# Kernel tuning notes

Measured on AMD Instinct MI355X. Metric: run time of the kernel, lower is better.

Reference implementation:

```python
import jax, jax.numpy as jnp
import numpy as np

N_NODES = 100000
N_EDGES = 1600000
NUM_FEATURES = 128
HIDDEN = 64
NUM_CLASSES = 2


def _gcn_norm(edge_index, num_nodes):
    # PyG gcn_norm: add self-loops, symmetric degree normalization.
    loop = jnp.arange(num_nodes, dtype=edge_index.dtype)
    src = jnp.concatenate([edge_index[0], loop])
    dst = jnp.concatenate([edge_index[1], loop])
    deg = jax.ops.segment_sum(jnp.ones_like(src, dtype=jnp.float32), dst,
                              num_segments=num_nodes)
    dinv = jnp.where(deg > 0, jax.lax.rsqrt(deg), 0.0)
    norm = dinv[src] * dinv[dst]  # [E + N]
    return src, dst, norm


def _gcn_conv(x, src, dst, norm, W, b, num_nodes):
    h = x @ W  # linear transform first (PyG GCNConv)
    msg = h[src] * norm[:, None]  # gather + edge scaling, [E+N, H]
    out = jax.ops.segment_sum(msg, dst, num_segments=num_nodes)  # scatter-add
    return out + b


def setup_inputs() -> dict:
    key = jax.random.key(0)
    ks = jax.random.split(key, 8)
    x = jax.random.normal(ks[0], (N_NODES, NUM_FEATURES), dtype=jnp.float32)
    edge_index = jax.random.randint(ks[1], (2, N_EDGES), 0, N_NODES, dtype=jnp.int32)
    def glorot(k, shape):
        lim = np.sqrt(6.0 / (shape[0] + shape[1]))
        return jax.random.uniform(k, shape, jnp.float32, -lim, lim)
    return {
        "x": x,
        "edge_index": edge_index,
        "W1": glorot(ks[2], (NUM_FEATURES, HIDDEN)),
        "b1": jnp.zeros((HIDDEN,), jnp.float32),
        "W2": glorot(ks[3], (HIDDEN, HIDDEN)),
        "b2": jnp.zeros((HIDDEN,), jnp.float32),
        "W3": glorot(ks[4], (HIDDEN, HIDDEN)),
        "b3": jnp.zeros((HIDDEN,), jnp.float32),
        "Wlin": glorot(ks[5], (HIDDEN, NUM_CLASSES)),
        "blin": jnp.zeros((NUM_CLASSES,), jnp.float32),
    }


def reference(x, edge_index, W1, b1, W2, b2, W3, b3, Wlin, blin):
    num_nodes = x.shape[0]
    src, dst, norm = _gcn_norm(edge_index, num_nodes)
    # eval mode: dropout is identity
    h = jax.nn.relu(_gcn_conv(x, src, dst, norm, W1, b1, num_nodes))
    h = jax.nn.relu(_gcn_conv(h, src, dst, norm, W2, b2, num_nodes))
    h = jax.nn.relu(_gcn_conv(h, src, dst, norm, W3, b3, num_nodes))
    logits = h @ Wlin + blin
    return jax.nn.log_softmax(logits, axis=1)
```

## Files before the change

kernel.cpp:

```cpp
#include <hip/hip_runtime.h>
#include <cstdint>
#include <cstddef>

#define NF 128
#define NH 64

typedef unsigned int uint32;

__device__ inline unsigned short f2bf(float f) {
  unsigned int u = __float_as_uint(f);
  return (unsigned short)((u + 0x7FFF + ((u >> 16) & 1)) >> 16);
}
__device__ inline float bf2f_lo(uint32 u) { return __uint_as_float(u << 16); }
__device__ inline float bf2f_hi(uint32 u) { return __uint_as_float(u & 0xFFFF0000u); }


__global__ __launch_bounds__(256) void count_kernel(const int* __restrict__ ei, int E,
                                                    int* __restrict__ cnt, int RW) {
  int pass = blockIdx.x & 7;
  int i = (blockIdx.x >> 3) * 256 + threadIdx.x;
  if (i * 4 >= E) return;
  int4 d = ((const int4*)(ei + E))[i];
  int lo = pass * RW, hi = lo + RW;
  if (d.x >= lo && d.x < hi) atomicAdd(&cnt[d.x], 1);
  if (d.y >= lo && d.y < hi) atomicAdd(&cnt[d.y], 1);
  if (d.z >= lo && d.z < hi) atomicAdd(&cnt[d.z], 1);
  if (d.w >= lo && d.w < hi) atomicAdd(&cnt[d.w], 1);
}

__global__ __launch_bounds__(256) void partial_kernel(const int* __restrict__ cnt, int N,
                                                      int* __restrict__ part) {
  __shared__ int sd[256];
  int t = threadIdx.x;
  int idx = blockIdx.x * 1024 + t * 4;
  int s = 0;
#pragma unroll
  for (int j = 0; j < 4; ++j)
    if (idx + j < N) s += cnt[idx + j];
  sd[t] = s;
  __syncthreads();
  for (int off = 128; off > 0; off >>= 1) {
    if (t < off) sd[t] += sd[t + off];
    __syncthreads();
  }
  if (t == 0) part[blockIdx.x] = sd[0];
}

__global__ __launch_bounds__(128) void scanp_kernel(int* __restrict__ part, int NB,
                                                    int* __restrict__ rowptrN) {
  __shared__ int s[128];
  int t = threadIdx.x;
  int v = (t < NB) ? part[t] : 0;
  s[t] = v;
  __syncthreads();
  for (int off = 1; off < 128; off <<= 1) {
    int add = (t >= off) ? s[t - off] : 0;
    __syncthreads();
    s[t] += add;
    __syncthreads();
  }
  if (t < NB) part[t] = s[t] - v;
  if (t == 0) rowptrN[0] = s[127];
}

__global__ __launch_bounds__(256) void rowptr_kernel(const int* __restrict__ cnt,
                                                     const int* __restrict__ part,
                                                     int* __restrict__ rowptr,
                                                     int* __restrict__ cnt2,
                                                     float* __restrict__ dinv, int N) {
  __shared__ int s[256];
  int t = threadIdx.x;
  int idx = blockIdx.x * 1024 + t * 4;
  int c[4];
  int ts = 0;
#pragma unroll
  for (int j = 0; j < 4; ++j) {
    c[j] = (idx + j < N) ? cnt[idx + j] : 0;
    ts += c[j];
  }
  s[t] = ts;
  __syncthreads();
  for (int off = 1; off < 256; off <<= 1) {
    int add = (t >= off) ? s[t - off] : 0;
    __syncthreads();
    s[t] += add;
    __syncthreads();
  }
  int run = s[t] - ts + part[blockIdx.x];
#pragma unroll
  for (int j = 0; j < 4; ++j) {
    if (idx + j < N) {
      rowptr[idx + j] = run;
      cnt2[idx + j] = run;
      dinv[idx + j] = rsqrtf((float)(c[j] + 1));
    }
    run += c[j];
  }
}

__global__ __launch_bounds__(256) void fill_kernel(const int* __restrict__ ei, int E,
                                                   int* __restrict__ cnt2,
                                                   const float* __restrict__ dinv,
                                                   int2* __restrict__ col2, int RW) {
  int pass = blockIdx.x & 7;
  int i = (blockIdx.x >> 3) * 256 + threadIdx.x;
  if (i * 4 >= E) return;
  int4 sv = ((const int4*)ei)[i];
  int4 dv = ((const int4*)(ei + E))[i];
  int lo = pass * RW, hi = lo + RW;
  int ss[4] = {sv.x, sv.y, sv.z, sv.w};
  int dd[4] = {dv.x, dv.y, dv.z, dv.w};
#pragma unroll
  for (int j = 0; j < 4; ++j) {
    int d = dd[j];
    if (d < lo || d >= hi) continue;
    int s = ss[j];
    float w = dinv[s] * dinv[d];
    int pos = atomicAdd(&cnt2[d], 1);
    col2[pos] = make_int2(s, __float_as_int(w));
  }
}


template <int K>
__global__ __launch_bounds__(256, 4) void gemm_kernel(const float* __restrict__ X,
                                                      const float* __restrict__ W,
                                                      uint32* __restrict__ Hb, int N) {
  __shared__ float XsT[64][68];
  __shared__ float Ws[64 * 64];
  const int tid = threadIdx.x;
  const int n0 = blockIdx.x * 64;
  const int tn = (tid >> 4) * 4;
  const int tf = (tid & 15) * 4;

  float acc[4][4];
#pragma unroll
  for (int i = 0; i < 4; ++i)
#pragma unroll
    for (int j = 0; j < 4; ++j) acc[i][j] = 0.f;

  for (int kt = 0; kt < K / 64; ++kt) {
    {
      const float4* Wg = (const float4*)(W + (size_t)kt * 64 * 64);
      float4* Wl = (float4*)Ws;
#pragma unroll
      for (int j = 0; j < 4; ++j) Wl[tid + j * 256] = Wg[tid + j * 256];
    }
#pragma unroll
    for (int j = 0; j < 4; ++j) {
      int idx = tid + j * 256;
      int n = idx >> 4;
      int kq = idx & 15;
      float4 v = make_float4(0.f, 0.f, 0.f, 0.f);
      if (n0 + n < N)
        v = *(const float4*)(X + (size_t)(n0 + n) * K + kt * 64 + kq * 4);
      XsT[kq * 4 + 0][n] = v.x;
      XsT[kq * 4 + 1][n] = v.y;
      XsT[kq * 4 + 2][n] = v.z;
      XsT[kq * 4 + 3][n] = v.w;
    }
    __syncthreads();
#pragma unroll 8
    for (int k = 0; k < 64; ++k) {
      float4 xv = *(const float4*)(&XsT[k][tn]);
      float4 wv = *(const float4*)(&Ws[k * 64 + tf]);
      acc[0][0] = fmaf(xv.x, wv.x, acc[0][0]);
      acc[0][1] = fmaf(xv.x, wv.y, acc[0][1]);
      acc[0][2] = fmaf(xv.x, wv.z, acc[0][2]);
      acc[0][3] = fmaf(xv.x, wv.w, acc[0][3]);
      acc[1][0] = fmaf(xv.y, wv.x, acc[1][0]);
      acc[1][1] = fmaf(xv.y, wv.y, acc[1][1]);
      acc[1][2] = fmaf(xv.y, wv.z, acc[1][2]);
      acc[1][3] = fmaf(xv.y, wv.w, acc[1][3]);
      acc[2][0] = fmaf(xv.z, wv.x, acc[2][0]);
      acc[2][1] = fmaf(xv.z, wv.y, acc[2][1]);
      acc[2][2] = fmaf(xv.z, wv.z, acc[2][2]);
      acc[2][3] = fmaf(xv.z, wv.w, acc[2][3]);
      acc[3][0] = fmaf(xv.w, wv.x, acc[3][0]);
      acc[3][1] = fmaf(xv.w, wv.y, acc[3][1]);
      acc[3][2] = fmaf(xv.w, wv.z, acc[3][2]);
      acc[3][3] = fmaf(xv.w, wv.w, acc[3][3]);
    }
    __syncthreads();
  }
#pragma unroll
  for (int i = 0; i < 4; ++i) {
    int n = n0 + tn + i;
    if (n < N) {
      uint32 p0 = (uint32)f2bf(acc[i][0]) | ((uint32)f2bf(acc[i][1]) << 16);
      uint32 p1 = (uint32)f2bf(acc[i][2]) | ((uint32)f2bf(acc[i][3]) << 16);
      *(uint2*)(Hb + (size_t)n * 32 + tf / 2) = make_uint2(p0, p1);
    }
  }
}

template <int FINAL>
__global__ __launch_bounds__(256) void prop_fused_kernel(
    const uint32* __restrict__ H32, const int* __restrict__ rowptr,
    const int2* __restrict__ col2, const float* __restrict__ dinv,
    const float* __restrict__ bias, const float* __restrict__ Wn,
    const float* __restrict__ blin, void* __restrict__ outv, int N) {
  __shared__ float Ws[64 * 64];
  __shared__ float rbuf[4][64];
  const int lane = threadIdx.x & 63;
  const int widx = threadIdx.x >> 6;
  const int fl = lane & 31;
  const int half = lane >> 5;

  if (!FINAL) {
    const float4* Wg = (const float4*)Wn;
    float4* Wl = (float4*)Ws;
    for (int i = threadIdx.x; i < 1024; i += 256) Wl[i] = Wg[i];
    __syncthreads();
  }

  int n = blockIdx.x * 4 + widx;
  n = __builtin_amdgcn_readfirstlane(n);
  if (n >= N) return;

  int e0 = rowptr[n];
  int e1 = rowptr[n + 1];
  float di = dinv[n];
  const int2* ec = col2 + e0;
  const int m = e1 - e0;

  float acc0 = 0.f, acc1 = 0.f;
  if (half == 0) {
    uint32 u = H32[(size_t)n * 32 + fl];
    float w = di * di;
    acc0 = bf2f_lo(u) * w;
    acc1 = bf2f_hi(u) * w;
  }

  const int npair = m >> 1;
  const int nfull = npair >> 3;
  for (int b = 0; b < nfull; ++b) {
    int s[8];
    float wv[8];
#pragma unroll
    for (int j = 0; j < 8; ++j) {
      int2 c = ec[2 * (b * 8 + j) + half];
      s[j] = c.x;
      wv[j] = __int_as_float(c.y);
    }
    uint32 u[8];
#pragma unroll
    for (int j = 0; j < 8; ++j) u[j] = H32[(size_t)s[j] * 32 + fl];
#pragma unroll
    for (int j = 0; j < 8; ++j) {
      acc0 = fmaf(wv[j], bf2f_lo(u[j]), acc0);
      acc1 = fmaf(wv[j], bf2f_hi(u[j]), acc1);
    }
  }
  for (int t = nfull * 8; t < npair; ++t) {
    int2 c = ec[2 * t + half];
    uint32 u = H32[(size_t)c.x * 32 + fl];
    float w = __int_as_float(c.y);
    acc0 = fmaf(w, bf2f_lo(u), acc0);
    acc1 = fmaf(w, bf2f_hi(u), acc1);
  }
  if ((m & 1) && half == 0) {
    int2 c = ec[m - 1];
    uint32 u = H32[(size_t)c.x * 32 + fl];
    float w = __int_as_float(c.y);
    acc0 = fmaf(w, bf2f_lo(u), acc0);
    acc1 = fmaf(w, bf2f_hi(u), acc1);
  }
  acc0 += __shfl_xor(acc0, 32, 64);
  acc1 += __shfl_xor(acc1, 32, 64);

  float2 bv = ((const float2*)bias)[fl];
  float r0 = acc0 + bv.x;
  float r1 = acc1 + bv.y;
  r0 = r0 > 0.f ? r0 : 0.f;
  r1 = r1 > 0.f ? r1 : 0.f;

  if (FINAL) {
    float t0 = 0.f, t1 = 0.f;
    if (half == 0) {
      t0 = r0 * Wn[4 * fl + 0] + r1 * Wn[4 * fl + 2];
      t1 = r0 * Wn[4 * fl + 1] + r1 * Wn[4 * fl + 3];
    }
#pragma unroll
    for (int off = 32; off > 0; off >>= 1) {
      t0 += __shfl_xor(t0, off, 64);
      t1 += __shfl_xor(t1, off, 64);
    }
    if (lane == 0) {
      float* out = (float*)outv;
      float l0 = t0 + blin[0];
      float l1 = t1 + blin[1];
      float mx = fmaxf(l0, l1);
      float lz = mx + logf(expf(l0 - mx) + expf(l1 - mx));
      out[(size_t)n * 2 + 0] = l0 - lz;
      out[(size_t)n * 2 + 1] = l1 - lz;
    }
  } else {
    if (half == 0) *(float2*)(&rbuf[widx][2 * fl]) = make_float2(r0, r1);
    __builtin_amdgcn_wave_barrier();
    float o = 0.f;
#pragma unroll
    for (int q = 0; q < 16; ++q) {
      float4 rv = *(const float4*)(&rbuf[widx][4 * q]);
      o = fmaf(rv.x, Ws[(4 * q + 0) * 64 + lane], o);
      o = fmaf(rv.y, Ws[(4 * q + 1) * 64 + lane], o);
      o = fmaf(rv.z, Ws[(4 * q + 2) * 64 + lane], o);
      o = fmaf(rv.w, Ws[(4 * q + 3) * 64 + lane], o);
    }
    ((unsigned short*)outv)[(size_t)n * 64 + lane] = f2bf(o);
  }
}


extern "C" void kernel_launch(void* const* d_in, const int* in_sizes, int n_in,
                              void* d_out, int out_size, void* d_ws, size_t ws_size,
                              hipStream_t stream) {
  const float* x  = (const float*)d_in[0];
  const int*   ei = (const int*)d_in[1];
  const float* W1 = (const float*)d_in[2];
  const float* b1 = (const float*)d_in[3];
  const float* W2 = (const float*)d_in[4];
  const float* b2 = (const float*)d_in[5];
  const float* W3 = (const float*)d_in[6];
  const float* b3 = (const float*)d_in[7];
  const float* Wl = (const float*)d_in[8];
  const float* bl = (const float*)d_in[9];
  float* out = (float*)d_out;

  const int N = in_sizes[0] / NF;
  const int E = in_sizes[1] / 2;

  char* w = (char*)d_ws;
  size_t off = 0;
  auto alloc = [&](size_t bytes) {
    void* p = w + off;
    off += bytes;
    off = (off + 15) & ~(size_t)15;
    return p;
  };
  int*    cnt    = (int*)alloc((size_t)N * 4);
  int*    cnt2   = (int*)alloc((size_t)N * 4);
  int*    rowptr = (int*)alloc((size_t)(N + 1) * 4);
  int*    part   = (int*)alloc(256 * 4);
  float*  dinv   = (float*)alloc((size_t)N * 4);
  int2*   col2   = (int2*)alloc((size_t)E * 8);
  uint32* hA     = (uint32*)alloc((size_t)N * 32 * 4);
  uint32* hB     = (uint32*)alloc((size_t)N * 32 * 4);

  const int NB = (N + 1023) / 1024;
  const int RW = (N + 7) / 8;
  const int NCHUNK = (E / 4 + 255) / 256;

  hipMemsetAsync(cnt, 0, (size_t)N * 4, stream);
  hipLaunchKernelGGL(count_kernel, dim3(8 * NCHUNK), dim3(256), 0, stream,
                     ei, E, cnt, RW);
  hipLaunchKernelGGL(partial_kernel, dim3(NB), dim3(256), 0, stream, cnt, N, part);
  hipLaunchKernelGGL(scanp_kernel, dim3(1), dim3(128), 0, stream, part, NB, rowptr + N);
  hipLaunchKernelGGL(rowptr_kernel, dim3(NB), dim3(256), 0, stream,
                     cnt, part, rowptr, cnt2, dinv, N);
  hipLaunchKernelGGL(fill_kernel, dim3(8 * NCHUNK), dim3(256), 0, stream,
                     ei, E, cnt2, dinv, col2, RW);

  hipLaunchKernelGGL(gemm_kernel<128>, dim3((N + 63) / 64), dim3(256), 0, stream,
                     x, W1, hA, N);
  hipLaunchKernelGGL(prop_fused_kernel<0>, dim3((N + 3) / 4), dim3(256), 0, stream,
                     hA, rowptr, col2, dinv, b1, W2, (const float*)nullptr, (void*)hB, N);
  hipLaunchKernelGGL(prop_fused_kernel<0>, dim3((N + 3) / 4), dim3(256), 0, stream,
                     hB, rowptr, col2, dinv, b2, W3, (const float*)nullptr, (void*)hA, N);
  hipLaunchKernelGGL(prop_fused_kernel<1>, dim3((N + 3) / 4), dim3(256), 0, stream,
                     hA, rowptr, col2, dinv, b3, Wl, bl, (void*)out, N);
}
```

Baseline: 444.9 us.

## Slice hidden features into 16-byte column planes and split aggregation from transform

The hidden matrix is stored as 8 feature slices of 8 bf16 values (16 bytes per node per slice), and aggregation blocks are interleaved by slice. Each slice is then ~1.6 MB, small enough to stay cache-resident while the random neighbor gathers run. The fused propagate+transform kernel is split into a separate aggregation kernel, a 64x64 transform GEMM kernel and a final log-softmax kernel. This trades extra launches, an extra intermediate round trip and 8x re-reading of the CSR edge list for better gather locality.

```diff
diff --git a/kernel.cpp b/kernel.cpp
--- a/kernel.cpp
+++ b/kernel.cpp
@@ -122,10 +122,11 @@
 }
 
 
+
 template <int K>
 __global__ __launch_bounds__(256, 4) void gemm_kernel(const float* __restrict__ X,
                                                       const float* __restrict__ W,
-                                                      uint32* __restrict__ Hb, int N) {
+                                                      uint32* __restrict__ Hs, int N) {
   __shared__ float XsT[64][68];
   __shared__ float Ws[64 * 64];
   const int tid = threadIdx.x;
@@ -183,131 +184,174 @@
     }
     __syncthreads();
   }
+  const int jj = tf >> 3;
+  const int q0 = (tf & 7) >> 1;
 #pragma unroll
   for (int i = 0; i < 4; ++i) {
     int n = n0 + tn + i;
     if (n < N) {
-      uint32 p0 = (uint32)f2bf(acc[i][0]) | ((uint32)f2bf(acc[i][1]) << 16);
-      uint32 p1 = (uint32)f2bf(acc[i][2]) | ((uint32)f2bf(acc[i][3]) << 16);
-      *(uint2*)(Hb + (size_t)n * 32 + tf / 2) = make_uint2(p0, p1);
-    }
-  }
-}
-
-template <int FINAL>
-__global__ __launch_bounds__(256) void prop_fused_kernel(
-    const uint32* __restrict__ H32, const int* __restrict__ rowptr,
+      uint32 a = (uint32)f2bf(acc[i][0]) | ((uint32)f2bf(acc[i][1]) << 16);
+      uint32 b = (uint32)f2bf(acc[i][2]) | ((uint32)f2bf(acc[i][3]) << 16);
+      *(uint2*)(Hs + (size_t)jj * N * 4 + (size_t)n * 4 + q0) = make_uint2(a, b);
+    }
+  }
+}
+
+__global__ __launch_bounds__(256) void agg_kernel(
+    const uint32* __restrict__ Hs, const int* __restrict__ rowptr,
     const int2* __restrict__ col2, const float* __restrict__ dinv,
-    const float* __restrict__ bias, const float* __restrict__ Wn,
-    const float* __restrict__ blin, void* __restrict__ outv, int N) {
-  __shared__ float Ws[64 * 64];
-  __shared__ float rbuf[4][64];
+    const float* __restrict__ bias, uint32* __restrict__ Rs, int N) {
+  const int slice = blockIdx.x & 7;
   const int lane = threadIdx.x & 63;
-  const int widx = threadIdx.x >> 6;
-  const int fl = lane & 31;
-  const int half = lane >> 5;
-
-  if (!FINAL) {
-    const float4* Wg = (const float4*)Wn;
-    float4* Wl = (float4*)Ws;
-    for (int i = threadIdx.x; i < 1024; i += 256) Wl[i] = Wg[i];
-    __syncthreads();
-  }
-
-  int n = blockIdx.x * 4 + widx;
-  n = __builtin_amdgcn_readfirstlane(n);
-  if (n >= N) return;
-
-  int e0 = rowptr[n];
-  int e1 = rowptr[n + 1];
-  float di = dinv[n];
-  const int2* ec = col2 + e0;
-  const int m = e1 - e0;
+  const int wv = threadIdx.x >> 6;
+  const int g = lane >> 4;
+  const int sub = (lane >> 2) & 3;
+  const int q = lane & 3;
+
+  int n = (blockIdx.x >> 3) * 16 + wv * 4 + g;
+  const bool nvalid = n < N;
+  const int ns = nvalid ? n : N - 1;
+  const int e0 = rowptr[ns];
+  const int m = nvalid ? (rowptr[ns + 1] - e0) : 0;
+  const uint32* Hj = Hs + (size_t)slice * N * 4;
 
   float acc0 = 0.f, acc1 = 0.f;
-  if (half == 0) {
-    uint32 u = H32[(size_t)n * 32 + fl];
-    float w = di * di;
-    acc0 = bf2f_lo(u) * w;
-    acc1 = bf2f_hi(u) * w;
-  }
-
-  const int npair = m >> 1;
-  const int nfull = npair >> 3;
-  for (int b = 0; b < nfull; ++b) {
-    int s[8];
-    float wv[8];
-#pragma unroll
-    for (int j = 0; j < 8; ++j) {
-      int2 c = ec[2 * (b * 8 + j) + half];
-      s[j] = c.x;
-      wv[j] = __int_as_float(c.y);
-    }
-    uint32 u[8];
-#pragma unroll
-    for (int j = 0; j < 8; ++j) u[j] = H32[(size_t)s[j] * 32 + fl];
-#pragma unroll
-    for (int j = 0; j < 8; ++j) {
-      acc0 = fmaf(wv[j], bf2f_lo(u[j]), acc0);
-      acc1 = fmaf(wv[j], bf2f_hi(u[j]), acc1);
-    }
-  }
-  for (int t = nfull * 8; t < npair; ++t) {
-    int2 c = ec[2 * t + half];
-    uint32 u = H32[(size_t)c.x * 32 + fl];
-    float w = __int_as_float(c.y);
+  int itmax = (m + 3) >> 2;
+  itmax = max(itmax, __shfl_xor(itmax, 16, 64));
+  itmax = max(itmax, __shfl_xor(itmax, 32, 64));
+  for (int it = 0; it < itmax; ++it) {
+    int er = it * 4 + sub;
+    bool v = er < m;
+    int e = v ? (e0 + er) : 0;
+    unsigned long long c =
+        __builtin_nontemporal_load((const unsigned long long*)col2 + e);
+    int src = (int)(c & 0xFFFFFFFFull);
+    float w = v ? __uint_as_float((uint32)(c >> 32)) : 0.f;
+    uint32 u = Hj[(size_t)src * 4 + q];
     acc0 = fmaf(w, bf2f_lo(u), acc0);
     acc1 = fmaf(w, bf2f_hi(u), acc1);
   }
-  if ((m & 1) && half == 0) {
-    int2 c = ec[m - 1];
-    uint32 u = H32[(size_t)c.x * 32 + fl];
-    float w = __int_as_float(c.y);
-    acc0 = fmaf(w, bf2f_lo(u), acc0);
-    acc1 = fmaf(w, bf2f_hi(u), acc1);
-  }
-  acc0 += __shfl_xor(acc0, 32, 64);
-  acc1 += __shfl_xor(acc1, 32, 64);
-
-  float2 bv = ((const float2*)bias)[fl];
+  acc0 += __shfl_xor(acc0, 4, 64);
+  acc0 += __shfl_xor(acc0, 8, 64);
+  acc1 += __shfl_xor(acc1, 4, 64);
+  acc1 += __shfl_xor(acc1, 8, 64);
+  float di = dinv[ns];
+  float d2 = di * di;
+  uint32 su = Hj[(size_t)ns * 4 + q];
+  acc0 = fmaf(d2, bf2f_lo(su), acc0);
+  acc1 = fmaf(d2, bf2f_hi(su), acc1);
+
+  float2 bv = ((const float2*)bias)[slice * 4 + q];
   float r0 = acc0 + bv.x;
   float r1 = acc1 + bv.y;
   r0 = r0 > 0.f ? r0 : 0.f;
   r1 = r1 > 0.f ? r1 : 0.f;
-
-  if (FINAL) {
-    float t0 = 0.f, t1 = 0.f;
-    if (half == 0) {
-      t0 = r0 * Wn[4 * fl + 0] + r1 * Wn[4 * fl + 2];
-      t1 = r0 * Wn[4 * fl + 1] + r1 * Wn[4 * fl + 3];
-    }
-#pragma unroll
-    for (int off = 32; off > 0; off >>= 1) {
-      t0 += __shfl_xor(t0, off, 64);
-      t1 += __shfl_xor(t1, off, 64);
-    }
-    if (lane == 0) {
-      float* out = (float*)outv;
-      float l0 = t0 + blin[0];
-      float l1 = t1 + blin[1];
-      float mx = fmaxf(l0, l1);
-      float lz = mx + logf(expf(l0 - mx) + expf(l1 - mx));
-      out[(size_t)n * 2 + 0] = l0 - lz;
-      out[(size_t)n * 2 + 1] = l1 - lz;
-    }
-  } else {
-    if (half == 0) *(float2*)(&rbuf[widx][2 * fl]) = make_float2(r0, r1);
-    __builtin_amdgcn_wave_barrier();
-    float o = 0.f;
-#pragma unroll
-    for (int q = 0; q < 16; ++q) {
-      float4 rv = *(const float4*)(&rbuf[widx][4 * q]);
-      o = fmaf(rv.x, Ws[(4 * q + 0) * 64 + lane], o);
-      o = fmaf(rv.y, Ws[(4 * q + 1) * 64 + lane], o);
-      o = fmaf(rv.z, Ws[(4 * q + 2) * 64 + lane], o);
-      o = fmaf(rv.w, Ws[(4 * q + 3) * 64 + lane], o);
-    }
-    ((unsigned short*)outv)[(size_t)n * 64 + lane] = f2bf(o);
+  if (nvalid && sub == 0) {
+    uint32 p = (uint32)f2bf(r0) | ((uint32)f2bf(r1) << 16);
+    __builtin_nontemporal_store(p, Rs + (size_t)slice * N * 4 + (size_t)n * 4 + q);
+  }
+}
+
+__global__ __launch_bounds__(256, 4) void transform_kernel(
+    const uint32* __restrict__ Rs, const float* __restrict__ W,
+    uint32* __restrict__ Hs, int N) {
+  __shared__ float XsT[64][68];
+  __shared__ float Ws[64 * 64];
+  const int tid = threadIdx.x;
+  const int n0 = blockIdx.x * 64;
+  const int tn = (tid >> 4) * 4;
+  const int tf = (tid & 15) * 4;
+  {
+    const float4* Wg = (const float4*)W;
+    float4* Wl = (float4*)Ws;
+#pragma unroll
+    for (int j = 0; j < 4; ++j) Wl[tid + j * 256] = Wg[tid + j * 256];
+  }
+#pragma unroll
+  for (int it = 0; it < 2; ++it) {
+    int sb = it * 256 + tid;
+    int n = sb & 63;
+    int j = sb >> 6;
+    uint4 v = make_uint4(0, 0, 0, 0);
+    if (n0 + n < N)
+      v = *(const uint4*)(Rs + (size_t)j * N * 4 + (size_t)(n0 + n) * 4);
+    XsT[j * 8 + 0][n] = bf2f_lo(v.x);
+    XsT[j * 8 + 1][n] = bf2f_hi(v.x);
+    XsT[j * 8 + 2][n] = bf2f_lo(v.y);
+    XsT[j * 8 + 3][n] = bf2f_hi(v.y);
+    XsT[j * 8 + 4][n] = bf2f_lo(v.z);
+    XsT[j * 8 + 5][n] = bf2f_hi(v.z);
+    XsT[j * 8 + 6][n] = bf2f_lo(v.w);
+    XsT[j * 8 + 7][n] = bf2f_hi(v.w);
+  }
+  __syncthreads();
+  float acc[4][4];
+#pragma unroll
+  for (int i = 0; i < 4; ++i)
+#pragma unroll
+    for (int j = 0; j < 4; ++j) acc[i][j] = 0.f;
+#pragma unroll 8
+  for (int k = 0; k < 64; ++k) {
+    float4 xv = *(const float4*)(&XsT[k][tn]);
+    float4 wv = *(const float4*)(&Ws[k * 64 + tf]);
+    acc[0][0] = fmaf(xv.x, wv.x, acc[0][0]);
+    acc[0][1] = fmaf(xv.x, wv.y, acc[0][1]);
+    acc[0][2] = fmaf(xv.x, wv.z, acc[0][2]);
+    acc[0][3] = fmaf(xv.x, wv.w, acc[0][3]);
+    acc[1][0] = fmaf(xv.y, wv.x, acc[1][0]);
+    acc[1][1] = fmaf(xv.y, wv.y, acc[1][1]);
+    acc[1][2] = fmaf(xv.y, wv.z, acc[1][2]);
+    acc[1][3] = fmaf(xv.y, wv.w, acc[1][3]);
+    acc[2][0] = fmaf(xv.z, wv.x, acc[2][0]);
+    acc[2][1] = fmaf(xv.z, wv.y, acc[2][1]);
+    acc[2][2] = fmaf(xv.z, wv.z, acc[2][2]);
+    acc[2][3] = fmaf(xv.z, wv.w, acc[2][3]);
+    acc[3][0] = fmaf(xv.w, wv.x, acc[3][0]);
+    acc[3][1] = fmaf(xv.w, wv.y, acc[3][1]);
+    acc[3][2] = fmaf(xv.w, wv.z, acc[3][2]);
+    acc[3][3] = fmaf(xv.w, wv.w, acc[3][3]);
+  }
+  const int jj = tf >> 3;
+  const int q0 = (tf & 7) >> 1;
+#pragma unroll
+  for (int i = 0; i < 4; ++i) {
+    int n = n0 + tn + i;
+    if (n < N) {
+      uint32 a = (uint32)f2bf(acc[i][0]) | ((uint32)f2bf(acc[i][1]) << 16);
+      uint32 b = (uint32)f2bf(acc[i][2]) | ((uint32)f2bf(acc[i][3]) << 16);
+      *(uint2*)(Hs + (size_t)jj * N * 4 + (size_t)n * 4 + q0) = make_uint2(a, b);
+    }
+  }
+}
+
+__global__ __launch_bounds__(256) void final_kernel(
+    const uint32* __restrict__ Rs, const float* __restrict__ Wlin,
+    const float* __restrict__ blin, float* __restrict__ out, int N) {
+  int lane = threadIdx.x & 63;
+  int n = blockIdx.x * 4 + (threadIdx.x >> 6);
+  if (n >= N) return;
+  float t0 = 0.f, t1 = 0.f;
+  if (lane < 32) {
+    int j = lane >> 2, q = lane & 3;
+    uint32 u = Rs[(size_t)j * N * 4 + (size_t)n * 4 + q];
+    float r0 = bf2f_lo(u), r1 = bf2f_hi(u);
+    int f0 = j * 8 + q * 2;
+    float4 wl = *(const float4*)(Wlin + f0 * 2);
+    t0 = r0 * wl.x + r1 * wl.z;
+    t1 = r0 * wl.y + r1 * wl.w;
+  }
+#pragma unroll
+  for (int off = 32; off > 0; off >>= 1) {
+    t0 += __shfl_xor(t0, off, 64);
+    t1 += __shfl_xor(t1, off, 64);
+  }
+  if (lane == 0) {
+    float l0 = t0 + blin[0];
+    float l1 = t1 + blin[1];
+    float mx = fmaxf(l0, l1);
+    float lz = mx + logf(expf(l0 - mx) + expf(l1 - mx));
+    out[(size_t)n * 2 + 0] = l0 - lz;
+    out[(size_t)n * 2 + 1] = l1 - lz;
   }
 }
 
@@ -344,12 +388,13 @@
   int*    part   = (int*)alloc(256 * 4);
   float*  dinv   = (float*)alloc((size_t)N * 4);
   int2*   col2   = (int2*)alloc((size_t)E * 8);
-  uint32* hA     = (uint32*)alloc((size_t)N * 32 * 4);
-  uint32* hB     = (uint32*)alloc((size_t)N * 32 * 4);
+  uint32* Hbuf   = (uint32*)alloc((size_t)N * 32 * 4);
+  uint32* Rbuf   = (uint32*)alloc((size_t)N * 32 * 4);
 
   const int NB = (N + 1023) / 1024;
   const int RW = (N + 7) / 8;
   const int NCHUNK = (E / 4 + 255) / 256;
+  const int AGGB = 8 * ((N + 15) / 16);
 
   hipMemsetAsync(cnt, 0, (size_t)N * 4, stream);
   hipLaunchKernelGGL(count_kernel, dim3(8 * NCHUNK), dim3(256), 0, stream,
@@ -362,11 +407,17 @@
                      ei, E, cnt2, dinv, col2, RW);
 
   hipLaunchKernelGGL(gemm_kernel<128>, dim3((N + 63) / 64), dim3(256), 0, stream,
-                     x, W1, hA, N);
-  hipLaunchKernelGGL(prop_fused_kernel<0>, dim3((N + 3) / 4), dim3(256), 0, stream,
-                     hA, rowptr, col2, dinv, b1, W2, (const float*)nullptr, (void*)hB, N);
-  hipLaunchKernelGGL(prop_fused_kernel<0>, dim3((N + 3) / 4), dim3(256), 0, stream,
-                     hB, rowptr, col2, dinv, b2, W3, (const float*)nullptr, (void*)hA, N);
-  hipLaunchKernelGGL(prop_fused_kernel<1>, dim3((N + 3) / 4), dim3(256), 0, stream,
-                     hA, rowptr, col2, dinv, b3, Wl, bl, (void*)out, N);
-}
+                     x, W1, Hbuf, N);
+  hipLaunchKernelGGL(agg_kernel, dim3(AGGB), dim3(256), 0, stream,
+                     Hbuf, rowptr, col2, dinv, b1, Rbuf, N);
+  hipLaunchKernelGGL(transform_kernel, dim3((N + 63) / 64), dim3(256), 0, stream,
+                     Rbuf, W2, Hbuf, N);
+  hipLaunchKernelGGL(agg_kernel, dim3(AGGB), dim3(256), 0, stream,
+                     Hbuf, rowptr, col2, dinv, b2, Rbuf, N);
+  hipLaunchKernelGGL(transform_kernel, dim3((N + 63) / 64), dim3(256), 0, stream,
+                     Rbuf, W3, Hbuf, N);
+  hipLaunchKernelGGL(agg_kernel, dim3(AGGB), dim3(256), 0, stream,
+                     Hbuf, rowptr, col2, dinv, b3, Rbuf, N);
+  hipLaunchKernelGGL(final_kernel, dim3((N + 3) / 4), dim3(256), 0, stream,
+                     Rbuf, Wl, bl, out, N);
+}
```

Result: slower. 759.0 us (+70.6%).

## Fuse first GEMM with degree counting and widen propagation edge parallelism

Applied to the files above, without the earlier changes.

The first-layer GEMM and the degree-count pass now run as one launch, with extra blocks appended to the grid for counting, so the two independent jobs can overlap and one launch disappears. The propagation kernel now handles four edges at a time per wave (16 lanes per edge, each loading a uint2 of features) instead of two, uses a predicated loop with no tail handling, and adds the self-loop after the cross-lane reduction. Edge-index and CSR loads use nontemporal hints. The fused GEMM/count blocks share one launch-bounds and LDS footprint, and the count blocks carry the GEMM's shared-memory allocation they do not use.

```diff
diff --git a/kernel.cpp b/kernel.cpp
--- a/kernel.cpp
+++ b/kernel.cpp
@@ -6,6 +6,7 @@
 #define NH 64
 
 typedef unsigned int uint32;
+typedef int int4v __attribute__((ext_vector_type(4)));
 
 __device__ inline unsigned short f2bf(float f) {
   unsigned int u = __float_as_uint(f);
@@ -15,123 +16,33 @@
 __device__ inline float bf2f_hi(uint32 u) { return __uint_as_float(u & 0xFFFF0000u); }
 
 
-__global__ __launch_bounds__(256) void count_kernel(const int* __restrict__ ei, int E,
-                                                    int* __restrict__ cnt, int RW) {
-  int pass = blockIdx.x & 7;
-  int i = (blockIdx.x >> 3) * 256 + threadIdx.x;
-  if (i * 4 >= E) return;
-  int4 d = ((const int4*)(ei + E))[i];
-  int lo = pass * RW, hi = lo + RW;
-  if (d.x >= lo && d.x < hi) atomicAdd(&cnt[d.x], 1);
-  if (d.y >= lo && d.y < hi) atomicAdd(&cnt[d.y], 1);
-  if (d.z >= lo && d.z < hi) atomicAdd(&cnt[d.z], 1);
-  if (d.w >= lo && d.w < hi) atomicAdd(&cnt[d.w], 1);
-}
-
-__global__ __launch_bounds__(256) void partial_kernel(const int* __restrict__ cnt, int N,
-                                                      int* __restrict__ part) {
-  __shared__ int sd[256];
-  int t = threadIdx.x;
-  int idx = blockIdx.x * 1024 + t * 4;
-  int s = 0;
-#pragma unroll
-  for (int j = 0; j < 4; ++j)
-    if (idx + j < N) s += cnt[idx + j];
-  sd[t] = s;
-  __syncthreads();
-  for (int off = 128; off > 0; off >>= 1) {
-    if (t < off) sd[t] += sd[t + off];
-    __syncthreads();
-  }
-  if (t == 0) part[blockIdx.x] = sd[0];
-}
-
-__global__ __launch_bounds__(128) void scanp_kernel(int* __restrict__ part, int NB,
-                                                    int* __restrict__ rowptrN) {
-  __shared__ int s[128];
-  int t = threadIdx.x;
-  int v = (t < NB) ? part[t] : 0;
-  s[t] = v;
-  __syncthreads();
-  for (int off = 1; off < 128; off <<= 1) {
-    int add = (t >= off) ? s[t - off] : 0;
-    __syncthreads();
-    s[t] += add;
-    __syncthreads();
-  }
-  if (t < NB) part[t] = s[t] - v;
-  if (t == 0) rowptrN[0] = s[127];
-}
-
-__global__ __launch_bounds__(256) void rowptr_kernel(const int* __restrict__ cnt,
-                                                     const int* __restrict__ part,
-                                                     int* __restrict__ rowptr,
-                                                     int* __restrict__ cnt2,
-                                                     float* __restrict__ dinv, int N) {
-  __shared__ int s[256];
-  int t = threadIdx.x;
-  int idx = blockIdx.x * 1024 + t * 4;
-  int c[4];
-  int ts = 0;
-#pragma unroll
-  for (int j = 0; j < 4; ++j) {
-    c[j] = (idx + j < N) ? cnt[idx + j] : 0;
-    ts += c[j];
-  }
-  s[t] = ts;
-  __syncthreads();
-  for (int off = 1; off < 256; off <<= 1) {
-    int add = (t >= off) ? s[t - off] : 0;
-    __syncthreads();
-    s[t] += add;
-    __syncthreads();
-  }
-  int run = s[t] - ts + part[blockIdx.x];
-#pragma unroll
-  for (int j = 0; j < 4; ++j) {
-    if (idx + j < N) {
-      rowptr[idx + j] = run;
-      cnt2[idx + j] = run;
-      dinv[idx + j] = rsqrtf((float)(c[j] + 1));
-    }
-    run += c[j];
-  }
-}
-
-__global__ __launch_bounds__(256) void fill_kernel(const int* __restrict__ ei, int E,
-                                                   int* __restrict__ cnt2,
-                                                   const float* __restrict__ dinv,
-                                                   int2* __restrict__ col2, int RW) {
-  int pass = blockIdx.x & 7;
-  int i = (blockIdx.x >> 3) * 256 + threadIdx.x;
-  if (i * 4 >= E) return;
-  int4 sv = ((const int4*)ei)[i];
-  int4 dv = ((const int4*)(ei + E))[i];
-  int lo = pass * RW, hi = lo + RW;
-  int ss[4] = {sv.x, sv.y, sv.z, sv.w};
-  int dd[4] = {dv.x, dv.y, dv.z, dv.w};
-#pragma unroll
-  for (int j = 0; j < 4; ++j) {
-    int d = dd[j];
-    if (d < lo || d >= hi) continue;
-    int s = ss[j];
-    float w = dinv[s] * dinv[d];
-    int pos = atomicAdd(&cnt2[d], 1);
-    col2[pos] = make_int2(s, __float_as_int(w));
-  }
-}
-
-
-template <int K>
-__global__ __launch_bounds__(256, 4) void gemm_kernel(const float* __restrict__ X,
-                                                      const float* __restrict__ W,
-                                                      uint32* __restrict__ Hb, int N) {
+__global__ __launch_bounds__(256, 4) void gemm1_count_kernel(
+    const float* __restrict__ X, const float* __restrict__ W,
+    uint32* __restrict__ Hb, int N,
+    const int* __restrict__ ei, int E, int* __restrict__ cnt, int RW, int G1) {
   __shared__ float XsT[64][68];
   __shared__ float Ws[64 * 64];
+
+  if ((int)blockIdx.x >= G1) {
+    int b = blockIdx.x - G1;
+    int pass = b & 7;
+    int i = (b >> 3) * 256 + threadIdx.x;
+    if (i * 4 >= E) return;
+    int4v d = __builtin_nontemporal_load(((const int4v*)(ei + E)) + i);
+    int lo = pass * RW, hi = lo + RW;
+    if (d.x >= lo && d.x < hi) atomicAdd(&cnt[d.x], 1);
+    if (d.y >= lo && d.y < hi) atomicAdd(&cnt[d.y], 1);
+    if (d.z >= lo && d.z < hi) atomicAdd(&cnt[d.z], 1);
+    if (d.w >= lo && d.w < hi) atomicAdd(&cnt[d.w], 1);
+    return;
+  }
+
   const int tid = threadIdx.x;
   const int n0 = blockIdx.x * 64;
+  if (n0 >= N) return;
   const int tn = (tid >> 4) * 4;
   const int tf = (tid & 15) * 4;
+  const int K = 128;
 
   float acc[4][4];
 #pragma unroll
@@ -194,18 +105,112 @@
   }
 }
 
+__global__ __launch_bounds__(256) void partial_kernel(const int* __restrict__ cnt, int N,
+                                                      int* __restrict__ part) {
+  __shared__ int sd[256];
+  int t = threadIdx.x;
+  int idx = blockIdx.x * 1024 + t * 4;
+  int s = 0;
+#pragma unroll
+  for (int j = 0; j < 4; ++j)
+    if (idx + j < N) s += cnt[idx + j];
+  sd[t] = s;
+  __syncthreads();
+  for (int off = 128; off > 0; off >>= 1) {
+    if (t < off) sd[t] += sd[t + off];
+    __syncthreads();
+  }
+  if (t == 0) part[blockIdx.x] = sd[0];
+}
+
+__global__ __launch_bounds__(128) void scanp_kernel(int* __restrict__ part, int NB,
+                                                    int* __restrict__ rowptrN) {
+  __shared__ int s[128];
+  int t = threadIdx.x;
+  int v = (t < NB) ? part[t] : 0;
+  s[t] = v;
+  __syncthreads();
+  for (int off = 1; off < 128; off <<= 1) {
+    int add = (t >= off) ? s[t - off] : 0;
+    __syncthreads();
+    s[t] += add;
+    __syncthreads();
+  }
+  if (t < NB) part[t] = s[t] - v;
+  if (t == 0) rowptrN[0] = s[127];
+}
+
+__global__ __launch_bounds__(256) void rowptr_kernel(const int* __restrict__ cnt,
+                                                     const int* __restrict__ part,
+                                                     int* __restrict__ rowptr,
+                                                     int* __restrict__ cnt2,
+                                                     float* __restrict__ dinv, int N) {
+  __shared__ int s[256];
+  int t = threadIdx.x;
+  int idx = blockIdx.x * 1024 + t * 4;
+  int c[4];
+  int ts = 0;
+#pragma unroll
+  for (int j = 0; j < 4; ++j) {
+    c[j] = (idx + j < N) ? cnt[idx + j] : 0;
+    ts += c[j];
+  }
+  s[t] = ts;
+  __syncthreads();
+  for (int off = 1; off < 256; off <<= 1) {
+    int add = (t >= off) ? s[t - off] : 0;
+    __syncthreads();
+    s[t] += add;
+    __syncthreads();
+  }
+  int run = s[t] - ts + part[blockIdx.x];
+#pragma unroll
+  for (int j = 0; j < 4; ++j) {
+    if (idx + j < N) {
+      rowptr[idx + j] = run;
+      cnt2[idx + j] = run;
+      dinv[idx + j] = rsqrtf((float)(c[j] + 1));
+    }
+    run += c[j];
+  }
+}
+
+__global__ __launch_bounds__(256) void fill_kernel(const int* __restrict__ ei, int E,
+                                                   int* __restrict__ cnt2,
+                                                   const float* __restrict__ dinv,
+                                                   int2* __restrict__ col2, int RW) {
+  int pass = blockIdx.x & 7;
+  int i = (blockIdx.x >> 3) * 256 + threadIdx.x;
+  if (i * 4 >= E) return;
+  int4v sv = __builtin_nontemporal_load(((const int4v*)ei) + i);
+  int4v dv = __builtin_nontemporal_load(((const int4v*)(ei + E)) + i);
+  int lo = pass * RW, hi = lo + RW;
+  int ss[4] = {sv.x, sv.y, sv.z, sv.w};
+  int dd[4] = {dv.x, dv.y, dv.z, dv.w};
+#pragma unroll
+  for (int j = 0; j < 4; ++j) {
+    int d = dd[j];
+    if (d < lo || d >= hi) continue;
+    int s = ss[j];
+    float w = dinv[s] * dinv[d];
+    int pos = atomicAdd(&cnt2[d], 1);
+    col2[pos] = make_int2(s, __float_as_int(w));
+  }
+}
+
+
 template <int FINAL>
 __global__ __launch_bounds__(256) void prop_fused_kernel(
     const uint32* __restrict__ H32, const int* __restrict__ rowptr,
     const int2* __restrict__ col2, const float* __restrict__ dinv,
     const float* __restrict__ bias, const float* __restrict__ Wn,
     const float* __restrict__ blin, void* __restrict__ outv, int N) {
-  __shared__ float Ws[64 * 64];
-  __shared__ float rbuf[4][64];
+  __shared__ float Ws[FINAL ? 4 : 64 * 64];
+  __shared__ float rbuf[FINAL ? 1 : 4][64];
   const int lane = threadIdx.x & 63;
   const int widx = threadIdx.x >> 6;
-  const int fl = lane & 31;
-  const int half = lane >> 5;
+  const int fq = lane & 15;
+  const int qtr = lane >> 4;
 
   if (!FINAL) {
     const float4* Wg = (const float4*)Wn;
@@ -218,68 +223,58 @@
   n = __builtin_amdgcn_readfirstlane(n);
   if (n >= N) return;
 
-  int e0 = rowptr[n];
-  int e1 = rowptr[n + 1];
-  float di = dinv[n];
-  const int2* ec = col2 + e0;
-  const int m = e1 - e0;
-
-  float acc0 = 0.f, acc1 = 0.f;
-  if (half == 0) {
-    uint32 u = H32[(size_t)n * 32 + fl];
-    float w = di * di;
-    acc0 = bf2f_lo(u) * w;
-    acc1 = bf2f_hi(u) * w;
-  }
-
-  const int npair = m >> 1;
-  const int nfull = npair >> 3;
-  for (int b = 0; b < nfull; ++b) {
-    int s[8];
-    float wv[8];
-#pragma unroll
-    for (int j = 0; j < 8; ++j) {
-      int2 c = ec[2 * (b * 8 + j) + half];
-      s[j] = c.x;
-      wv[j] = __int_as_float(c.y);
-    }
-    uint32 u[8];
-#pragma unroll
-    for (int j = 0; j < 8; ++j) u[j] = H32[(size_t)s[j] * 32 + fl];
-#pragma unroll
-    for (int j = 0; j < 8; ++j) {
-      acc0 = fmaf(wv[j], bf2f_lo(u[j]), acc0);
-      acc1 = fmaf(wv[j], bf2f_hi(u[j]), acc1);
-    }
-  }
-  for (int t = nfull * 8; t < npair; ++t) {
-    int2 c = ec[2 * t + half];
-    uint32 u = H32[(size_t)c.x * 32 + fl];
-    float w = __int_as_float(c.y);
-    acc0 = fmaf(w, bf2f_lo(u), acc0);
-    acc1 = fmaf(w, bf2f_hi(u), acc1);
-  }
-  if ((m & 1) && half == 0) {
-    int2 c = ec[m - 1];
-    uint32 u = H32[(size_t)c.x * 32 + fl];
-    float w = __int_as_float(c.y);
-    acc0 = fmaf(w, bf2f_lo(u), acc0);
-    acc1 = fmaf(w, bf2f_hi(u), acc1);
-  }
+  const int e0 = rowptr[n];
+  const int m = rowptr[n + 1] - e0;
+  const unsigned long long* ecs = (const unsigned long long*)(col2 + e0);
+
+  float acc0 = 0.f, acc1 = 0.f, acc2 = 0.f, acc3 = 0.f;
+  const int nq = (m + 3) >> 2;
+  for (int it = 0; it < nq; ++it) {
+    int er = it * 4 + qtr;
+    bool v = er < m;
+    unsigned long long c = __builtin_nontemporal_load(ecs + (v ? er : 0));
+    int src = (int)(c & 0xFFFFFFFFull);
+    float w = v ? __uint_as_float((uint32)(c >> 32)) : 0.f;
+    uint2 u = *(const uint2*)(H32 + (size_t)src * 32 + fq * 2);
+    acc0 = fmaf(w, bf2f_lo(u.x), acc0);
+    acc1 = fmaf(w, bf2f_hi(u.x), acc1);
+    acc2 = fmaf(w, bf2f_lo(u.y), acc2);
+    acc3 = fmaf(w, bf2f_hi(u.y), acc3);
+  }
+  acc0 += __shfl_xor(acc0, 16, 64);
+  acc1 += __shfl_xor(acc1, 16, 64);
+  acc2 += __shfl_xor(acc2, 16, 64);
+  acc3 += __shfl_xor(acc3, 16, 64);
   acc0 += __shfl_xor(acc0, 32, 64);
   acc1 += __shfl_xor(acc1, 32, 64);
-
-  float2 bv = ((const float2*)bias)[fl];
+  acc2 += __shfl_xor(acc2, 32, 64);
+  acc3 += __shfl_xor(acc3, 32, 64);
+
+  float di = dinv[n];
+  float d2 = di * di;
+  uint2 su = *(const uint2*)(H32 + (size_t)n * 32 + fq * 2);
+  acc0 = fmaf(d2, bf2f_lo(su.x), acc0);
+  acc1 = fmaf(d2, bf2f_hi(su.x), acc1);
+  acc2 = fmaf(d2, bf2f_lo(su.y), acc2);
+  acc3 = fmaf(d2, bf2f_hi(su.y), acc3);
+
+  float4 bv = *(const float4*)(bias + fq * 4);
   float r0 = acc0 + bv.x;
   float r1 = acc1 + bv.y;
+  float r2 = acc2 + bv.z;
+  float r3 = acc3 + bv.w;
   r0 = r0 > 0.f ? r0 : 0.f;
   r1 = r1 > 0.f ? r1 : 0.f;
+  r2 = r2 > 0.f ? r2 : 0.f;
+  r3 = r3 > 0.f ? r3 : 0.f;
 
   if (FINAL) {
     float t0 = 0.f, t1 = 0.f;
-    if (half == 0) {
-      t0 = r0 * Wn[4 * fl + 0] + r1 * Wn[4 * fl + 2];
-      t1 = r0 * Wn[4 * fl + 1] + r1 * Wn[4 * fl + 3];
+    if (qtr == 0) {
+      float4 wa = ((const float4*)Wn)[2 * fq];
+      float4 wb = ((const float4*)Wn)[2 * fq + 1];
+      t0 = r0 * wa.x + r1 * wa.z + r2 * wb.x + r3 * wb.z;
+      t1 = r0 * wa.y + r1 * wa.w + r2 * wb.y + r3 * wb.w;
     }
 #pragma unroll
     for (int off = 32; off > 0; off >>= 1) {
@@ -296,7 +291,7 @@
       out[(size_t)n * 2 + 1] = l1 - lz;
     }
   } else {
-    if (half == 0) *(float2*)(&rbuf[widx][2 * fl]) = make_float2(r0, r1);
+    if (qtr == 0) *(float4*)(&rbuf[widx][4 * fq]) = make_float4(r0, r1, r2, r3);
     __builtin_amdgcn_wave_barrier();
     float o = 0.f;
 #pragma unroll
@@ -350,10 +345,11 @@
   const int NB = (N + 1023) / 1024;
   const int RW = (N + 7) / 8;
   const int NCHUNK = (E / 4 + 255) / 256;
+  const int G1 = ((((N + 63) / 64) + 7) / 8) * 8;
 
   hipMemsetAsync(cnt, 0, (size_t)N * 4, stream);
-  hipLaunchKernelGGL(count_kernel, dim3(8 * NCHUNK), dim3(256), 0, stream,
-                     ei, E, cnt, RW);
+  hipLaunchKernelGGL(gemm1_count_kernel, dim3(G1 + 8 * NCHUNK), dim3(256), 0, stream,
+                     x, W1, hA, N, ei, E, cnt, RW, G1);
   hipLaunchKernelGGL(partial_kernel, dim3(NB), dim3(256), 0, stream, cnt, N, part);
   hipLaunchKernelGGL(scanp_kernel, dim3(1), dim3(128), 0, stream, part, NB, rowptr + N);
   hipLaunchKernelGGL(rowptr_kernel, dim3(NB), dim3(256), 0, stream,
@@ -361,8 +357,6 @@
   hipLaunchKernelGGL(fill_kernel, dim3(8 * NCHUNK), dim3(256), 0, stream,
                      ei, E, cnt2, dinv, col2, RW);
 
-  hipLaunchKernelGGL(gemm_kernel<128>, dim3((N + 63) / 64), dim3(256), 0, stream,
-                     x, W1, hA, N);
   hipLaunchKernelGGL(prop_fused_kernel<0>, dim3((N + 3) / 4), dim3(256), 0, stream,
                      hA, rowptr, col2, dinv, b1, W2, (const float*)nullptr, (void*)hB, N);
   hipLaunchKernelGGL(prop_fused_kernel<0>, dim3((N + 3) / 4), dim3(256), 0, stream,
```

Measured after the change: 476.4 us. 1.07x slower.
